# Performance work log

Measured on AMD Instinct MI355X. Metric: run time of the kernel, lower is better.

Reference implementation:

```python
import jax, jax.numpy as jnp
import numpy as np
from jax import lax

B, C, H, W = 4, 64, 256, 256
CH = C // 2  # attention hidden channels


def conv2d_same(x, w, b):
    # x: [B,Ci,H,W], w: [Co,Ci,kh,kw]
    y = lax.conv_general_dilated(x, w, (1, 1), 'SAME',
                                 dimension_numbers=('NCHW', 'OIHW', 'NCHW'))
    return y + b[None, :, None, None]


def conv1x1(x, w):
    # w: [Co,Ci]
    return jnp.einsum('oi,bihw->bohw', w, x)


def irnn_scan(x, w, b, axis, reverse):
    """Directional IRNN: h_t = relu(x_t + w_c * h_{t-1} + b_c), per channel.
    axis: 2 (rows/H) or 3 (cols/W). reverse=True scans from the far edge
    (e.g. bottom-to-top for 'up', right-to-left for 'left')."""
    xs = jnp.moveaxis(x, axis, 0)            # [L, B, C, rest]
    wb = w[None, :, None]                    # broadcast over [B, C, rest]
    bb = b[None, :, None]

    def step(h, xt):
        h = jax.nn.relu(xt + wb * h + bb)
        return h, h

    h0 = jnp.zeros_like(xs[0])
    _, ys = lax.scan(step, h0, xs, reverse=reverse)
    return jnp.moveaxis(ys, 0, axis)


def setup_inputs() -> dict:
    key = jax.random.key(0)
    ks = jax.random.split(key, 16)
    d = {}
    d['x'] = jax.random.normal(ks[0], (B, C, H, W), dtype=jnp.float32)
    # conv_in: 1x1, no bias
    d['w_in'] = jax.random.normal(ks[1], (C, C), dtype=jnp.float32) * 0.05
    # IRNN depthwise 1x1 weights (init alpha=1.0 in torch) + biases
    for i, name in enumerate(['up', 'right', 'down', 'left']):
        d['w_' + name] = jnp.ones((C,), dtype=jnp.float32)
        d['b_' + name] = jax.random.normal(ks[2 + i], (C,), dtype=jnp.float32) * 0.01
    # convD2: 1x1, 4C -> C, no bias
    d['wD2'] = jax.random.normal(ks[6], (C, 4 * C), dtype=jnp.float32) * 0.01
    # attention layers
    d['a1_w'] = jax.random.normal(ks[7], (CH, C, 3, 3), dtype=jnp.float32) * 0.05
    d['a1_b'] = jnp.zeros((CH,), dtype=jnp.float32)
    d['a2_w'] = jax.random.normal(ks[8], (CH, CH, 3, 3), dtype=jnp.float32) * 0.05
    d['a2_b'] = jnp.zeros((CH,), dtype=jnp.float32)
    d['a3_w'] = jax.random.normal(ks[9], (1, CH), dtype=jnp.float32) * 0.05
    d['a3_b'] = jnp.zeros((1,), dtype=jnp.float32)
    return d


def reference(x, w_in, w_up, b_up, w_right, b_right, w_down, b_down,
              w_left, b_left, wD2, a1_w, a1_b, a2_w, a2_b, a3_w, a3_b):
    out = conv1x1(x, w_in)
    # four directional spatial IRNN scans
    top_up = irnn_scan(out, w_up, b_up, axis=2, reverse=True)     # bottom->top
    top_right = irnn_scan(out, w_right, b_right, axis=3, reverse=False)  # left->right
    top_down = irnn_scan(out, w_down, b_down, axis=2, reverse=False)     # top->bottom
    top_left = irnn_scan(out, w_left, b_left, axis=3, reverse=True)      # right->left
    cat = jnp.concatenate([top_up, top_right, top_down, top_left], axis=1)  # [B,4C,H,W]
    out = jax.nn.relu(conv1x1(cat, wD2))
    # attention gate
    a = jax.nn.relu(conv2d_same(out, a1_w, a1_b))
    a = jax.nn.relu(conv2d_same(a, a2_w, a2_b))
    a = conv1x1(a, a3_w) + a3_b[None, :, None, None]
    weight = jax.nn.sigmoid(a)                # [B,1,H,W]
    return jax.nn.relu(x * weight)
```

## Files before the change

kernel.cpp:

```cpp
#include <hip/hip_runtime.h>
#include <hip/hip_bf16.h>

#define HWSZ  65536

typedef unsigned short ushort_t;
typedef unsigned int   uint_t;
typedef __attribute__((ext_vector_type(8))) _Float16 half8;
typedef __attribute__((ext_vector_type(2))) _Float16 half2v;
typedef __attribute__((ext_vector_type(4))) float f32x4;

static __device__ __forceinline__ void gl_lds16(const void* g, void* l) {
    __builtin_amdgcn_global_load_lds(
        (const __attribute__((address_space(1))) unsigned int*)g,
        (__attribute__((address_space(3))) unsigned int*)l, 16, 0, 0);
}

__global__ __launch_bounds__(256) void k1_mfma(
    const float* __restrict__ x, const float* __restrict__ w_in,
    _Float16* __restrict__ out0)
{
    __shared__ _Float16 ah[64][72];
    __shared__ _Float16 al[64][72];
    int b   = blockIdx.x >> 10;
    int hw0 = (blockIdx.x & 1023) << 6;
    const float* xb = x + ((size_t)b * 64) * HWSZ + hw0;
    int wave = threadIdx.x >> 6, lane = threadIdx.x & 63;
    int n16 = lane & 15, quad = lane >> 4;

    half8 Bh[2], Bl[2];
#pragma unroll
    for (int s = 0; s < 2; s++) {
        const float* wp = w_in + (wave * 16 + n16) * 64 + s * 32 + quad * 8;
#pragma unroll
        for (int j = 0; j < 8; j++) {
            float v = wp[j];
            _Float16 h = (_Float16)v;
            float r = v - (float)h;
            Bh[s][j] = h; Bl[s][j] = (_Float16)r;
        }
    }

    {
        int px  = threadIdx.x & 63;
        int ic0 = (threadIdx.x >> 6) << 4;
        const float* cp = xb + (size_t)ic0 * HWSZ + px;
        float v[16];
#pragma unroll
        for (int e = 0; e < 16; e++)
            v[e] = cp[(size_t)e * HWSZ];
        half8 h0, h1, l0, l1;
#pragma unroll
        for (int e = 0; e < 8; e++) {
            _Float16 h = (_Float16)v[e];
            h0[e] = h; l0[e] = (_Float16)(v[e] - (float)h);
        }
#pragma unroll
        for (int e = 0; e < 8; e++) {
            _Float16 h = (_Float16)v[8 + e];
            h1[e] = h; l1[e] = (_Float16)(v[8 + e] - (float)h);
        }
        *(half8*)&ah[px][ic0]     = h0;
        *(half8*)&ah[px][ic0 + 8] = h1;
        *(half8*)&al[px][ic0]     = l0;
        *(half8*)&al[px][ic0 + 8] = l1;
    }
    __syncthreads();

    f32x4 acc[4] = {};
#pragma unroll
    for (int j = 0; j < 4; j++) {
        int px = j * 16 + n16;
#pragma unroll
        for (int s = 0; s < 2; s++) {
            half8 Ah = *(const half8*)&ah[px][s * 32 + quad * 8];
            half8 Al = *(const half8*)&al[px][s * 32 + quad * 8];
            acc[j] = __builtin_amdgcn_mfma_f32_16x16x32_f16(Ah, Bh[s], acc[j], 0, 0, 0);
            acc[j] = __builtin_amdgcn_mfma_f32_16x16x32_f16(Al, Bh[s], acc[j], 0, 0, 0);
            acc[j] = __builtin_amdgcn_mfma_f32_16x16x32_f16(Ah, Bl[s], acc[j], 0, 0, 0);
        }
    }
    _Float16* ob = out0 + ((size_t)b * HWSZ + hw0) * 64 + wave * 16;
#pragma unroll
    for (int j = 0; j < 4; j++)
#pragma unroll
        for (int r = 0; r < 4; r++) {
            int px = j * 16 + quad * 4 + r;
            ob[(size_t)px * 64 + n16] = (_Float16)acc[j][r];
        }
}

__global__ __launch_bounds__(256) void k2_scan(
    const _Float16* __restrict__ out0,
    const float* __restrict__ w_up, const float* __restrict__ b_up,
    const float* __restrict__ w_rt, const float* __restrict__ b_rt,
    const float* __restrict__ w_dn, const float* __restrict__ b_dn,
    const float* __restrict__ w_lf, const float* __restrict__ b_lf,
    _Float16* __restrict__ cat)
{
    int c2 = threadIdx.x & 31;
    int q  = threadIdx.x >> 5;
    int dir = blockIdx.x >> 7;
    int bid = blockIdx.x & 127;
    int b = bid >> 5, g = bid & 31;
    int line = g * 8 + q;
    size_t base = (size_t)b * HWSZ;
    bool vert = dir < 2;
    bool rev  = dir & 1;

    const float *wp, *bp; int coff;
    if      (dir == 0) { wp = w_dn; bp = b_dn; coff = 128; }
    else if (dir == 1) { wp = w_up; bp = b_up; coff = 0;   }
    else if (dir == 2) { wp = w_rt; bp = b_rt; coff = 64;  }
    else               { wp = w_lf; bp = b_lf; coff = 192; }
    float w0v = wp[2 * c2], b0v = bp[2 * c2];
    float w1v = wp[2 * c2 + 1], b1v = bp[2 * c2 + 1];
    int coff2 = coff >> 1;

    const half2v* src = (const half2v*)out0;
    half2v* dst = (half2v*)cat;

    float h0 = 0.f, h1 = 0.f;
    for (int k0 = 0; k0 < 256; k0 += 16) {
        half2v v[16];
#pragma unroll
        for (int jx = 0; jx < 16; jx++) {
            int i = rev ? 255 - (k0 + jx) : (k0 + jx);
            size_t pix = vert ? (base + i * 256 + line) : (base + line * 256 + i);
            v[jx] = src[pix * 32 + c2];
        }
#pragma unroll
        for (int jx = 0; jx < 16; jx++) {
            int i = rev ? 255 - (k0 + jx) : (k0 + jx);
            size_t pix = vert ? (base + i * 256 + line) : (base + line * 256 + i);
            h0 = fmaxf(0.f, (float)v[jx][0] + w0v * h0 + b0v);
            h1 = fmaxf(0.f, (float)v[jx][1] + w1v * h1 + b1v);
            half2v o; o[0] = (_Float16)h0; o[1] = (_Float16)h1;
            dst[pix * 128 + coff2 + c2] = o;
        }
    }
}

__global__ __launch_bounds__(256) void packall(
    const float* __restrict__ wD2, const float* __restrict__ a1w,
    const float* __restrict__ a2w,
    _Float16* __restrict__ wf, _Float16* __restrict__ p1,
    _Float16* __restrict__ p2)
{
    int i = blockIdx.x * 256 + threadIdx.x;
    if (i < 16384) {
        wf[i] = (_Float16)wD2[i];
        return;
    }
    int k = i - 16384;
    if (k < 18432) {
        int j = k & 7, lane = (k >> 3) & 63, st = k >> 9;
        int s = st >> 1, t = st & 1;
        int oc = t * 16 + (lane & 15);
        int gk = s * 32 + (lane >> 4) * 8 + j;
        int dydx = gk >> 6, ic = gk & 63;
        p1[k] = (_Float16)a1w[((oc * 64 + ic) * 3 + dydx / 3) * 3 + dydx % 3];
    } else if (k < 27648) {
        int e = k - 18432;
        int j = e & 7, lane = (e >> 3) & 63, st = e >> 9;
        int s = st >> 1, t = st & 1;
        int oc = t * 16 + (lane & 15);
        int gk = s * 32 + (lane >> 4) * 8 + j;
        int dydx = gk >> 5, ic = gk & 31;
        p2[e] = (_Float16)a2w[((oc * 32 + ic) * 3 + dydx / 3) * 3 + dydx % 3];
    }
}

__global__ __launch_bounds__(256) void k3_mfma(
    const _Float16* __restrict__ cat, const _Float16* __restrict__ wf,
    _Float16* __restrict__ out3)
{
    __shared__ _Float16 As[64 * 256];
    int wave = threadIdx.x >> 6, lane = threadIdx.x & 63;
    int n16 = lane & 15, quad = lane >> 4;
    size_t p0 = (size_t)blockIdx.x * 64;

    half8 B[8];
#pragma unroll
    for (int s = 0; s < 8; s++)
        B[s] = *(const half8*)(wf + (size_t)(wave * 16 + n16) * 256 + s * 32 + quad * 8);

#pragma unroll
    for (int it = 0; it < 8; it++) {
        int px = wave * 16 + it * 2 + (lane >> 5);
        int pu = lane & 31;
        int lu = pu ^ (px & 7);
        const _Float16* gp = cat + ((p0 + px) << 8) + lu * 8;
        _Float16* lp = As + wave * 4096 + it * 512;
        gl_lds16(gp, lp);
    }
    __syncthreads();

    f32x4 acc[4] = {};
#pragma unroll
    for (int j = 0; j < 4; j++) {
        int px = j * 16 + n16;
        const _Float16* lrow = As + px * 256;
        int x7 = px & 7;
#pragma unroll
        for (int s = 0; s < 8; s++) {
            int phys = (s * 4 + quad) ^ x7;
            half8 a = *(const half8*)(lrow + phys * 8);
            acc[j] = __builtin_amdgcn_mfma_f32_16x16x32_f16(a, B[s], acc[j], 0, 0, 0);
        }
    }

#pragma unroll
    for (int j = 0; j < 4; j++)
#pragma unroll
        for (int r = 0; r < 4; r++) {
            size_t op = (p0 + j * 16 + quad * 4 + r) * 64 + wave * 16 + n16;
            out3[op] = (_Float16)fmaxf(acc[j][r], 0.f);
        }
}

template <int IC, bool GATE>
__global__ __launch_bounds__(256) void convmfma(
    const _Float16* __restrict__ in, const _Float16* __restrict__ pb,
    const float* __restrict__ bias, _Float16* __restrict__ oh,
    const float* __restrict__ a3w, const float* __restrict__ a3b,
    float* __restrict__ gbuf)
{
    constexpr int UPX = IC / 8;
    constexpr int KST = IC / 32;
    constexpr int PPS = 64 / UPX;
    __shared__ _Float16 Ls[6 * 66 * IC];

    int wave = threadIdx.x >> 6, lane = threadIdx.x & 63;
    int n16 = lane & 15, quad = lane >> 4;
    int bid = blockIdx.x;
    int bb  = bid >> 8;
    int hh0 = ((bid >> 2) & 63) << 2;
    int w0  = (bid & 3) << 6;
    const _Float16* ib = in + (size_t)bb * HWSZ * IC;

#pragma unroll
    for (int it = 0; it < (6 * UPX) / 4; it++) {
        int q   = it * 4 + wave;
        int r   = q / UPX, seg = q % UPX;
        int gh  = hh0 - 1 + r;
        int pxr = seg * PPS + lane / UPX;
        int pu  = lane % UPX;
        int px_lin = r * 66 + 1 + pxr;
        int lu  = (UPX == 8) ? (pu ^ (px_lin & 7)) : pu;
        _Float16* lp = Ls + (size_t)(r * 66 + 1 + seg * PPS) * IC;
        if ((unsigned)gh < 256u) {
            const _Float16* gp = ib + ((size_t)(gh * 256 + w0 + pxr)) * IC + lu * 8;
            gl_lds16(gp, lp);
        } else {
            half8 z = {};
            *(half8*)(lp + (size_t)lane * 8) = z;
        }
    }
    if (threadIdx.x < 12 * UPX) {
        int pu = threadIdx.x % UPX;
        int ph = threadIdx.x / UPX;
        int r = ph >> 1, side = ph & 1;
        int col = side ? 65 : 0;
        int gh = hh0 - 1 + r;
        int gw = w0 - 1 + side * 65;
        int px_lin = r * 66 + col;
        int lu = (UPX == 8) ? (pu ^ (px_lin & 7)) : pu;
        half8 v = {};
        if ((unsigned)gh < 256u && (unsigned)gw < 256u)
            v = *(const half8*)(ib + ((size_t)(gh * 256 + gw)) * IC + lu * 8);
        *(half8*)(Ls + (size_t)px_lin * IC + pu * 8) = v;
    }
    __syncthreads();

    f32x4 acc[4][2] = {};
#pragma unroll
    for (int dydx = 0; dydx < 9; dydx++) {
        int dy = dydx / 3, dx = dydx % 3;
        int r_lds = wave + dy;
#pragma unroll
        for (int kst = 0; kst < KST; kst++) {
            int s = dydx * KST + kst;
            half8 B0 = *(const half8*)(pb + (size_t)((s * 2 + 0) * 64 + lane) * 8);
            half8 B1 = *(const half8*)(pb + (size_t)((s * 2 + 1) * 64 + lane) * 8);
            int u = kst * 4 + quad;
#pragma unroll
            for (int j = 0; j < 4; j++) {
                int px_lin = r_lds * 66 + j * 16 + n16 + dx;
                int phys = (UPX == 8) ? (u ^ (px_lin & 7)) : u;
                half8 A = *(const half8*)(Ls + (size_t)px_lin * IC + phys * 8);
                acc[j][0] = __builtin_amdgcn_mfma_f32_16x16x32_f16(A, B0, acc[j][0], 0, 0, 0);
                acc[j][1] = __builtin_amdgcn_mfma_f32_16x16x32_f16(A, B1, acc[j][1], 0, 0, 0);
            }
        }
    }

    int hh = hh0 + wave;
    if constexpr (GATE) {
        float bv0 = bias[n16], bv1 = bias[16 + n16];
        float aw0 = a3w[n16], aw1 = a3w[16 + n16];
        float ab  = a3b[0];
#pragma unroll
        for (int j = 0; j < 4; j++)
#pragma unroll
            for (int r = 0; r < 4; r++) {
                float r0 = fmaxf(acc[j][0][r] + bv0, 0.f);
                float r1 = fmaxf(acc[j][1][r] + bv1, 0.f);
                float sv = fmaf(aw0, r0, aw1 * r1);
                sv += __shfl_xor(sv, 1, 16);
                sv += __shfl_xor(sv, 2, 16);
                sv += __shfl_xor(sv, 4, 16);
                sv += __shfl_xor(sv, 8, 16);
                if (n16 == 0) {
                    float gg = 1.f / (1.f + __expf(-(sv + ab)));
                    gbuf[(size_t)bb * HWSZ + hh * 256 + w0 + j * 16 + quad * 4 + r] = gg;
                }
            }
    } else {
#pragma unroll
        for (int t = 0; t < 2; t++) {
            float bv = bias[t * 16 + n16];
#pragma unroll
            for (int j = 0; j < 4; j++)
#pragma unroll
                for (int r = 0; r < 4; r++) {
                    int wp = w0 + j * 16 + quad * 4 + r;
                    size_t op = ((size_t)bb * HWSZ + hh * 256 + wp) * 32 + t * 16 + n16;
                    oh[op] = (_Float16)fmaxf(acc[j][t][r] + bv, 0.f);
                }
        }
    }
}

__global__ __launch_bounds__(256) void k6b(
    const float* __restrict__ x, const float* __restrict__ gbuf,
    float* __restrict__ out)
{
    const float4* x4 = (const float4*)x;
    const float4* g4 = (const float4*)gbuf;
    float4* o4 = (float4*)out;
    size_t base = (size_t)blockIdx.x * 2048;
#pragma unroll
    for (int k = 0; k < 8; k++) {
        size_t e = base + k * 256 + threadIdx.x;
        int plane = (int)(e >> 14);
        int hw4   = (int)(e & 16383);
        int b     = plane >> 6;
        float4 xv = x4[e];
        float4 gv = g4[(size_t)b * 16384 + hw4];
        float4 ov;
        ov.x = fmaxf(0.f, xv.x * gv.x);
        ov.y = fmaxf(0.f, xv.y * gv.y);
        ov.z = fmaxf(0.f, xv.z * gv.z);
        ov.w = fmaxf(0.f, xv.w * gv.w);
        o4[e] = ov;
    }
}

extern "C" void kernel_launch(void* const* d_in, const int* in_sizes, int n_in,
                              void* d_out, int out_size, void* d_ws, size_t ws_size,
                              hipStream_t stream)
{
    const float* x     = (const float*)d_in[0];
    const float* w_in  = (const float*)d_in[1];
    const float* w_up  = (const float*)d_in[2];
    const float* b_up  = (const float*)d_in[3];
    const float* w_rt  = (const float*)d_in[4];
    const float* b_rt  = (const float*)d_in[5];
    const float* w_dn  = (const float*)d_in[6];
    const float* b_dn  = (const float*)d_in[7];
    const float* w_lf  = (const float*)d_in[8];
    const float* b_lf  = (const float*)d_in[9];
    const float* wD2   = (const float*)d_in[10];
    const float* a1w   = (const float*)d_in[11];
    const float* a1b   = (const float*)d_in[12];
    const float* a2w   = (const float*)d_in[13];
    const float* a2b   = (const float*)d_in[14];
    const float* a3w   = (const float*)d_in[15];
    const float* a3b   = (const float*)d_in[16];
    float* out = (float*)d_out;

    char* ws = (char*)d_ws;
    _Float16* out0 = (_Float16*)ws;
    _Float16* out3 = (_Float16*)ws;
    _Float16* wf16 = (_Float16*)(ws + (33ull << 20));
    _Float16* p1   = (_Float16*)(ws + (34ull << 20));
    _Float16* p2   = (_Float16*)(ws + (35ull << 20));
    float*    gbuf = (float*)   (ws + (36ull << 20));
    _Float16* cat  = (_Float16*)(ws + (64ull << 20));
    _Float16* a1   = (_Float16*)(ws + (64ull << 20));

    k1_mfma   <<<4096, 256, 0, stream>>>(x, w_in, out0);
    k2_scan   <<<512,  256, 0, stream>>>(out0, w_up, b_up, w_rt, b_rt,
                                         w_dn, b_dn, w_lf, b_lf, cat);
    packall   <<<172,  256, 0, stream>>>(wD2, a1w, a2w, wf16, p1, p2);
    k3_mfma   <<<4096, 256, 0, stream>>>(cat, wf16, out3);
    convmfma<64, false><<<1024, 256, 0, stream>>>(out3, p1, a1b, a1,
                                                  nullptr, nullptr, nullptr);
    convmfma<32, true> <<<1024, 256, 0, stream>>>(a1, p2, a2b, nullptr,
                                                  a3w, a3b, gbuf);
    k6b       <<<2048, 256, 0, stream>>>(x, gbuf, out);
}
```

Measured before the change: 266.2 us.

## Fuse gate multiply into second conv and fold weight packing into k1

The sigmoid gate is staged in shared memory and the final relu(x*gate) is computed inside the gated conv kernel, which removes the gbuf round-trip and the separate elementwise kernel. Weight packing moves into extra blocks of the first kernel, saving one launch. The trade-off is that the conv kernel now streams 64 channels of x and out with scalar per-channel loads and stores, which may cut its occupancy or bandwidth efficiency.

```diff
diff --git a/kernel.cpp b/kernel.cpp
--- a/kernel.cpp
+++ b/kernel.cpp
@@ -17,8 +17,38 @@
 
 __global__ __launch_bounds__(256) void k1_mfma(
     const float* __restrict__ x, const float* __restrict__ w_in,
-    _Float16* __restrict__ out0)
-{
+    _Float16* __restrict__ out0,
+    const float* __restrict__ wD2, const float* __restrict__ a1w,
+    const float* __restrict__ a2w,
+    _Float16* __restrict__ wf, _Float16* __restrict__ p1,
+    _Float16* __restrict__ p2)
+{
+    if (blockIdx.x >= 4096) {
+        int i = (blockIdx.x - 4096) * 256 + threadIdx.x;
+        if (i < 16384) {
+            wf[i] = (_Float16)wD2[i];
+        } else {
+            int k = i - 16384;
+            if (k < 18432) {
+                int j = k & 7, lane = (k >> 3) & 63, st = k >> 9;
+                int s = st >> 1, t = st & 1;
+                int oc = t * 16 + (lane & 15);
+                int gk = s * 32 + (lane >> 4) * 8 + j;
+                int dydx = gk >> 6, ic = gk & 63;
+                p1[k] = (_Float16)a1w[((oc * 64 + ic) * 3 + dydx / 3) * 3 + dydx % 3];
+            } else if (k < 27648) {
+                int e = k - 18432;
+                int j = e & 7, lane = (e >> 3) & 63, st = e >> 9;
+                int s = st >> 1, t = st & 1;
+                int oc = t * 16 + (lane & 15);
+                int gk = s * 32 + (lane >> 4) * 8 + j;
+                int dydx = gk >> 5, ic = gk & 31;
+                p2[e] = (_Float16)a2w[((oc * 32 + ic) * 3 + dydx / 3) * 3 + dydx % 3];
+            }
+        }
+        return;
+    }
+
     __shared__ _Float16 ah[64][72];
     __shared__ _Float16 al[64][72];
     int b   = blockIdx.x >> 10;
@@ -140,36 +170,6 @@
     }
 }
 
-__global__ __launch_bounds__(256) void packall(
-    const float* __restrict__ wD2, const float* __restrict__ a1w,
-    const float* __restrict__ a2w,
-    _Float16* __restrict__ wf, _Float16* __restrict__ p1,
-    _Float16* __restrict__ p2)
-{
-    int i = blockIdx.x * 256 + threadIdx.x;
-    if (i < 16384) {
-        wf[i] = (_Float16)wD2[i];
-        return;
-    }
-    int k = i - 16384;
-    if (k < 18432) {
-        int j = k & 7, lane = (k >> 3) & 63, st = k >> 9;
-        int s = st >> 1, t = st & 1;
-        int oc = t * 16 + (lane & 15);
-        int gk = s * 32 + (lane >> 4) * 8 + j;
-        int dydx = gk >> 6, ic = gk & 63;
-        p1[k] = (_Float16)a1w[((oc * 64 + ic) * 3 + dydx / 3) * 3 + dydx % 3];
-    } else if (k < 27648) {
-        int e = k - 18432;
-        int j = e & 7, lane = (e >> 3) & 63, st = e >> 9;
-        int s = st >> 1, t = st & 1;
-        int oc = t * 16 + (lane & 15);
-        int gk = s * 32 + (lane >> 4) * 8 + j;
-        int dydx = gk >> 5, ic = gk & 31;
-        p2[e] = (_Float16)a2w[((oc * 32 + ic) * 3 + dydx / 3) * 3 + dydx % 3];
-    }
-}
-
 __global__ __launch_bounds__(256) void k3_mfma(
     const _Float16* __restrict__ cat, const _Float16* __restrict__ wf,
     _Float16* __restrict__ out3)
@@ -223,12 +223,13 @@
     const _Float16* __restrict__ in, const _Float16* __restrict__ pb,
     const float* __restrict__ bias, _Float16* __restrict__ oh,
     const float* __restrict__ a3w, const float* __restrict__ a3b,
-    float* __restrict__ gbuf)
+    const float* __restrict__ x, float* __restrict__ out)
 {
     constexpr int UPX = IC / 8;
     constexpr int KST = IC / 32;
     constexpr int PPS = 64 / UPX;
     __shared__ _Float16 Ls[6 * 66 * IC];
+    __shared__ float gtile[4][64];
 
     int wave = threadIdx.x >> 6, lane = threadIdx.x & 63;
     int n16 = lane & 15, quad = lane >> 4;
@@ -310,11 +311,19 @@
                 sv += __shfl_xor(sv, 2, 16);
                 sv += __shfl_xor(sv, 4, 16);
                 sv += __shfl_xor(sv, 8, 16);
-                if (n16 == 0) {
-                    float gg = 1.f / (1.f + __expf(-(sv + ab)));
-                    gbuf[(size_t)bb * HWSZ + hh * 256 + w0 + j * 16 + quad * 4 + r] = gg;
-                }
+                if (n16 == 0)
+                    gtile[wave][j * 16 + quad * 4 + r] =
+                        1.f / (1.f + __expf(-(sv + ab)));
             }
+        __syncthreads();
+        int row = threadIdx.x >> 6;
+        int px  = threadIdx.x & 63;
+        float gg = gtile[row][px];
+        const float* xb2 = x + ((size_t)bb * 64) * HWSZ + (hh0 + row) * 256 + w0 + px;
+        float* ob2 = out + ((size_t)bb * 64) * HWSZ + (hh0 + row) * 256 + w0 + px;
+#pragma unroll 8
+        for (int c = 0; c < 64; c++)
+            ob2[(size_t)c * HWSZ] = fmaxf(0.f, xb2[(size_t)c * HWSZ] * gg);
     } else {
 #pragma unroll
         for (int t = 0; t < 2; t++) {
@@ -328,31 +337,6 @@
                     oh[op] = (_Float16)fmaxf(acc[j][t][r] + bv, 0.f);
                 }
         }
-    }
-}
-
-__global__ __launch_bounds__(256) void k6b(
-    const float* __restrict__ x, const float* __restrict__ gbuf,
-    float* __restrict__ out)
-{
-    const float4* x4 = (const float4*)x;
-    const float4* g4 = (const float4*)gbuf;
-    float4* o4 = (float4*)out;
-    size_t base = (size_t)blockIdx.x * 2048;
-#pragma unroll
-    for (int k = 0; k < 8; k++) {
-        size_t e = base + k * 256 + threadIdx.x;
-        int plane = (int)(e >> 14);
-        int hw4   = (int)(e & 16383);
-        int b     = plane >> 6;
-        float4 xv = x4[e];
-        float4 gv = g4[(size_t)b * 16384 + hw4];
-        float4 ov;
-        ov.x = fmaxf(0.f, xv.x * gv.x);
-        ov.y = fmaxf(0.f, xv.y * gv.y);
-        ov.z = fmaxf(0.f, xv.z * gv.z);
-        ov.w = fmaxf(0.f, xv.w * gv.w);
-        o4[e] = ov;
     }
 }
 
@@ -385,18 +369,16 @@
     _Float16* wf16 = (_Float16*)(ws + (33ull << 20));
     _Float16* p1   = (_Float16*)(ws + (34ull << 20));
     _Float16* p2   = (_Float16*)(ws + (35ull << 20));
-    float*    gbuf = (float*)   (ws + (36ull << 20));
     _Float16* cat  = (_Float16*)(ws + (64ull << 20));
     _Float16* a1   = (_Float16*)(ws + (64ull << 20));
 
-    k1_mfma   <<<4096, 256, 0, stream>>>(x, w_in, out0);
+    k1_mfma   <<<4268, 256, 0, stream>>>(x, w_in, out0, wD2, a1w, a2w,
+                                         wf16, p1, p2);
     k2_scan   <<<512,  256, 0, stream>>>(out0, w_up, b_up, w_rt, b_rt,
                                          w_dn, b_dn, w_lf, b_lf, cat);
-    packall   <<<172,  256, 0, stream>>>(wD2, a1w, a2w, wf16, p1, p2);
     k3_mfma   <<<4096, 256, 0, stream>>>(cat, wf16, out3);
     convmfma<64, false><<<1024, 256, 0, stream>>>(out3, p1, a1b, a1,
-                                                  nullptr, nullptr, nullptr);
+                                                  nullptr, nullptr, nullptr, nullptr);
     convmfma<32, true> <<<1024, 256, 0, stream>>>(a1, p2, a2b, nullptr,
-                                                  a3w, a3b, gbuf);
-    k6b       <<<2048, 256, 0, stream>>>(x, gbuf, out);
-}
+                                                  a3w, a3b, x, out);
+}
```

Result: faster. 260.6 us (-2.1%).
